# Kernel optimization log

Hardware: AMD Instinct MI355X
Metric: run time of the kernel (lower is better)

Reference implementation:

```python
import jax, jax.numpy as jnp
import numpy as np

N_NODES = 50000
N_EDGES = 1600000
IN_CH = 128
HID = 128
LAT = 32


def _sage_conv(h, src, dst, W_l, W_r, b, num_nodes):
    # PyG SAGEConv: mean-aggregate neighbor (source) features at dst,
    # then lin_l(aggr) + lin_r(x) + bias
    msg = h[src]                                             # [E, d] irregular gather
    agg = jax.ops.segment_sum(msg, dst, num_segments=num_nodes)
    cnt = jax.ops.segment_sum(jnp.ones((src.shape[0], 1), h.dtype), dst,
                              num_segments=num_nodes)
    mean = agg / jnp.maximum(cnt, 1.0)
    return mean @ W_l + h @ W_r + b


def setup_inputs() -> dict:
    key = jax.random.key(0)
    ks = jax.random.split(key, 16)
    s = 0.05
    inp = {
        "x": jax.random.normal(ks[0], (N_NODES, IN_CH), jnp.float32),
        "edge_index": jax.random.randint(ks[1], (2, N_EDGES), 0, N_NODES, jnp.int32),
        "eps": jax.random.normal(ks[2], (N_NODES, LAT), jnp.float32),
        # SAGEConv layer 0
        "Wl0": jax.random.normal(ks[3], (IN_CH, HID), jnp.float32) * s,
        "Wr0": jax.random.normal(ks[4], (IN_CH, HID), jnp.float32) * s,
        "b0": jnp.zeros((HID,), jnp.float32),
        # SAGEConv layer 1
        "Wl1": jax.random.normal(ks[5], (HID, HID), jnp.float32) * s,
        "Wr1": jax.random.normal(ks[6], (HID, HID), jnp.float32) * s,
        "b1": jnp.zeros((HID,), jnp.float32),
        # mu / logvar heads
        "Wmu": jax.random.normal(ks[7], (HID, LAT), jnp.float32) * s,
        "bmu": jnp.zeros((LAT,), jnp.float32),
        "Wlv": jax.random.normal(ks[8], (HID, LAT), jnp.float32) * s,
        "blv": jnp.zeros((LAT,), jnp.float32),
    }
    return inp


def reference(x, edge_index, eps, Wl0, Wr0, b0, Wl1, Wr1, b1, Wmu, bmu, Wlv, blv):
    src, dst = edge_index[0], edge_index[1]
    n = x.shape[0]
    h = jax.nn.relu(_sage_conv(x, src, dst, Wl0, Wr0, b0, n))
    h = jax.nn.relu(_sage_conv(h, src, dst, Wl1, Wr1, b1, n))
    mu = h @ Wmu + bmu
    logvar = h @ Wlv + blv
    z = mu + eps * jnp.exp(0.5 * logvar)          # reparameterize
    probs = jax.nn.sigmoid(jnp.sum(z[src] * z[dst], axis=-1))  # edge decode
    return probs, mu, logvar
```

## Files before the change

### kernel.cpp

```cpp
#include <hip/hip_runtime.h>
#include <math.h>

#define NN 50000
#define NE 1600000
#define CH 128
#define LAT 32
#define NB 196

__device__ __forceinline__ unsigned short f2bf(float f) {
  unsigned int u = __float_as_uint(f);
  unsigned int r = u + 0x7FFFu + ((u >> 16) & 1u);
  return (unsigned short)(r >> 16);
}
__device__ __forceinline__ float bf2f(unsigned short s) {
  return __uint_as_float(((unsigned int)s) << 16);
}

__global__ void k_tobf16(const float* __restrict__ in, unsigned short* __restrict__ out,
                         int n4) {
  int i = blockIdx.x * 256 + threadIdx.x;
  if (i < n4) {
    float4 v = reinterpret_cast<const float4*>(in)[i];
    ushort4 o;
    o.x = f2bf(v.x); o.y = f2bf(v.y); o.z = f2bf(v.z); o.w = f2bf(v.w);
    reinterpret_cast<ushort4*>(out)[i] = o;
  }
}

__global__ void k_hist(const int* __restrict__ dst, int* __restrict__ deg) {
  int e = blockIdx.x * 256 + threadIdx.x;
  if (e < NE) atomicAdd(&deg[dst[e]], 1);
}

__global__ void k_scan1(const int* __restrict__ deg, int* __restrict__ bsum) {
  __shared__ int red[256];
  int i = blockIdx.x * 256 + threadIdx.x;
  red[threadIdx.x] = (i < NN) ? deg[i] : 0;
  __syncthreads();
  for (int s = 128; s > 0; s >>= 1) {
    if (threadIdx.x < s) red[threadIdx.x] += red[threadIdx.x + s];
    __syncthreads();
  }
  if (threadIdx.x == 0) bsum[blockIdx.x] = red[0];
}

__global__ void k_scan2(const int* __restrict__ bsum, int* __restrict__ boff) {
  __shared__ int tmp[256];
  int t = threadIdx.x;
  int v = (t < NB) ? bsum[t] : 0;
  tmp[t] = v;
  __syncthreads();
  for (int off = 1; off < 256; off <<= 1) {
    int add = (t >= off) ? tmp[t - off] : 0;
    __syncthreads();
    tmp[t] += add;
    __syncthreads();
  }
  if (t < NB) boff[t] = tmp[t] - v;
}

__global__ void k_scan3(const int* __restrict__ deg, const int* __restrict__ boff,
                        int* __restrict__ row_start, int* __restrict__ cursor) {
  __shared__ int tmp[256];
  int t = threadIdx.x;
  int i = blockIdx.x * 256 + t;
  int v = (i < NN) ? deg[i] : 0;
  tmp[t] = v;
  __syncthreads();
  for (int off = 1; off < 256; off <<= 1) {
    int add = (t >= off) ? tmp[t - off] : 0;
    __syncthreads();
    tmp[t] += add;
    __syncthreads();
  }
  int excl = tmp[t] - v + boff[blockIdx.x];
  if (i < NN) { row_start[i] = excl; cursor[i] = excl; }
}

__global__ void k_fill(const int* __restrict__ src, const int* __restrict__ dst,
                       int* __restrict__ cursor, int* __restrict__ eid) {
  int e = blockIdx.x * 256 + threadIdx.x;
  if (e < NE) {
    int d = dst[e];
    int pos = atomicAdd(&cursor[d], 1);
    eid[pos] = src[e];
  }
}

__global__ __launch_bounds__(256) void k_sage2(
    const unsigned short* __restrict__ featb, const float* __restrict__ feat32,
    const int* __restrict__ deg, const int* __restrict__ row_start,
    const int* __restrict__ eid,
    const float* __restrict__ Wl, const float* __restrict__ Wr,
    const float* __restrict__ bias,
    float* __restrict__ outf, unsigned short* __restrict__ outb) {
  __shared__ float mean_s[32][128];
  __shared__ float h_s[32][128];
  int tid = threadIdx.x;
  int nbase = blockIdx.x * 32;
  int hw = tid >> 5, q = tid & 31;

  for (int n = hw; n < 32; n += 8) {
    int v = nbase + n;
    float ax = 0.f, ay = 0.f, az = 0.f, aw = 0.f;
    float4 hh = make_float4(0.f, 0.f, 0.f, 0.f);
    if (v < NN) {
      int r0 = row_start[v];
      int dg = deg[v];
      int i = 0;
      for (; i + 3 < dg; i += 4) {
        int s0 = eid[r0 + i + 0];
        int s1 = eid[r0 + i + 1];
        int s2 = eid[r0 + i + 2];
        int s3 = eid[r0 + i + 3];
        ushort4 a = *reinterpret_cast<const ushort4*>(featb + (size_t)s0 * CH + q * 4);
        ushort4 b = *reinterpret_cast<const ushort4*>(featb + (size_t)s1 * CH + q * 4);
        ushort4 c = *reinterpret_cast<const ushort4*>(featb + (size_t)s2 * CH + q * 4);
        ushort4 d = *reinterpret_cast<const ushort4*>(featb + (size_t)s3 * CH + q * 4);
        ax += bf2f(a.x) + bf2f(b.x) + bf2f(c.x) + bf2f(d.x);
        ay += bf2f(a.y) + bf2f(b.y) + bf2f(c.y) + bf2f(d.y);
        az += bf2f(a.z) + bf2f(b.z) + bf2f(c.z) + bf2f(d.z);
        aw += bf2f(a.w) + bf2f(b.w) + bf2f(c.w) + bf2f(d.w);
      }
      for (; i < dg; ++i) {
        int s0 = eid[r0 + i];
        ushort4 a = *reinterpret_cast<const ushort4*>(featb + (size_t)s0 * CH + q * 4);
        ax += bf2f(a.x); ay += bf2f(a.y); az += bf2f(a.z); aw += bf2f(a.w);
      }
      float r = 1.0f / (float)max(dg, 1);
      ax *= r; ay *= r; az *= r; aw *= r;
      if (feat32) {
        hh = *reinterpret_cast<const float4*>(feat32 + (size_t)v * CH + q * 4);
      } else {
        ushort4 hb = *reinterpret_cast<const ushort4*>(featb + (size_t)v * CH + q * 4);
        hh = make_float4(bf2f(hb.x), bf2f(hb.y), bf2f(hb.z), bf2f(hb.w));
      }
    }
    *reinterpret_cast<float4*>(&mean_s[n][q * 4]) = make_float4(ax, ay, az, aw);
    *reinterpret_cast<float4*>(&h_s[n][q * 4]) = hh;
  }
  __syncthreads();

  int jg = tid & 31, ng = tid >> 5;
  int j0 = jg * 4, nl = ng * 4;
  float acc[4][4];
#pragma unroll
  for (int a = 0; a < 4; a++)
#pragma unroll
    for (int b = 0; b < 4; b++) acc[a][b] = 0.f;

#pragma unroll 4
  for (int k = 0; k < 128; ++k) {
    float4 wl = *reinterpret_cast<const float4*>(Wl + k * CH + j0);
    float4 wr = *reinterpret_cast<const float4*>(Wr + k * CH + j0);
#pragma unroll
    for (int n = 0; n < 4; ++n) {
      float m = mean_s[nl + n][k];
      float hv = h_s[nl + n][k];
      acc[n][0] += m * wl.x + hv * wr.x;
      acc[n][1] += m * wl.y + hv * wr.y;
      acc[n][2] += m * wl.z + hv * wr.z;
      acc[n][3] += m * wl.w + hv * wr.w;
    }
  }

  float4 bb = *reinterpret_cast<const float4*>(bias + j0);
#pragma unroll
  for (int n = 0; n < 4; ++n) {
    int v = nbase + nl + n;
    if (v < NN) {
      float4 o;
      o.x = fmaxf(acc[n][0] + bb.x, 0.f);
      o.y = fmaxf(acc[n][1] + bb.y, 0.f);
      o.z = fmaxf(acc[n][2] + bb.z, 0.f);
      o.w = fmaxf(acc[n][3] + bb.w, 0.f);
      if (outf) *reinterpret_cast<float4*>(outf + (size_t)v * CH + j0) = o;
      if (outb) {
        ushort4 ob;
        ob.x = f2bf(o.x); ob.y = f2bf(o.y); ob.z = f2bf(o.z); ob.w = f2bf(o.w);
        *reinterpret_cast<ushort4*>(outb + (size_t)v * CH + j0) = ob;
      }
    }
  }
}

__global__ __launch_bounds__(256) void k_heads(
    const float* __restrict__ h2, const float* __restrict__ eps,
    const float* __restrict__ Wmu, const float* __restrict__ bmu,
    const float* __restrict__ Wlv, const float* __restrict__ blv,
    float* __restrict__ mu_out, float* __restrict__ lv_out,
    float* __restrict__ z) {
  __shared__ float hs[32][132];
  int tid = threadIdx.x;
  int nbase = blockIdx.x * 32;

  for (int f = tid; f < 1024; f += 256) {
    int row = f >> 5;
    int c4 = (f & 31) * 4;
    int v = nbase + row;
    float4 hh = make_float4(0.f, 0.f, 0.f, 0.f);
    if (v < NN) hh = *reinterpret_cast<const float4*>(h2 + (size_t)v * CH + c4);
    *reinterpret_cast<float4*>(&hs[row][c4]) = hh;
  }
  __syncthreads();

  int n = tid >> 3;
  int j0 = (tid & 7) * 4;
  float am[4] = {0.f, 0.f, 0.f, 0.f};
  float al[4] = {0.f, 0.f, 0.f, 0.f};
#pragma unroll 4
  for (int k = 0; k < 128; ++k) {
    float4 wm = *reinterpret_cast<const float4*>(Wmu + k * LAT + j0);
    float4 wv = *reinterpret_cast<const float4*>(Wlv + k * LAT + j0);
    float hv = hs[n][k];
    am[0] += hv * wm.x; am[1] += hv * wm.y; am[2] += hv * wm.z; am[3] += hv * wm.w;
    al[0] += hv * wv.x; al[1] += hv * wv.y; al[2] += hv * wv.z; al[3] += hv * wv.w;
  }
  int v = nbase + n;
  if (v < NN) {
    float4 bm = *reinterpret_cast<const float4*>(bmu + j0);
    float4 bl = *reinterpret_cast<const float4*>(blv + j0);
    float4 e4 = *reinterpret_cast<const float4*>(eps + (size_t)v * LAT + j0);
    float4 mu, lv, zz;
    mu.x = am[0] + bm.x; mu.y = am[1] + bm.y; mu.z = am[2] + bm.z; mu.w = am[3] + bm.w;
    lv.x = al[0] + bl.x; lv.y = al[1] + bl.y; lv.z = al[2] + bl.z; lv.w = al[3] + bl.w;
    zz.x = mu.x + e4.x * expf(0.5f * lv.x);
    zz.y = mu.y + e4.y * expf(0.5f * lv.y);
    zz.z = mu.z + e4.z * expf(0.5f * lv.z);
    zz.w = mu.w + e4.w * expf(0.5f * lv.w);
    *reinterpret_cast<float4*>(mu_out + (size_t)v * LAT + j0) = mu;
    *reinterpret_cast<float4*>(lv_out + (size_t)v * LAT + j0) = lv;
    *reinterpret_cast<float4*>(z + (size_t)v * LAT + j0) = zz;
  }
}

__global__ void k_decode(const int* __restrict__ src, const int* __restrict__ dst,
                         const float* __restrict__ z, float* __restrict__ probs) {
  int t = blockIdx.x * 256 + threadIdx.x;
  int e = t >> 3, part = t & 7;
  if (e >= NE) return;
  int s = src[e], d = dst[e];
  float4 a = *reinterpret_cast<const float4*>(z + (size_t)s * LAT + part * 4);
  float4 b = *reinterpret_cast<const float4*>(z + (size_t)d * LAT + part * 4);
  float p = a.x * b.x + a.y * b.y + a.z * b.z + a.w * b.w;
  p += __shfl_xor(p, 1);
  p += __shfl_xor(p, 2);
  p += __shfl_xor(p, 4);
  if (part == 0) probs[e] = 1.0f / (1.0f + expf(-p));
}

extern "C" void kernel_launch(void* const* d_in, const int* in_sizes, int n_in,
                              void* d_out, int out_size, void* d_ws, size_t ws_size,
                              hipStream_t stream) {
  const float* x   = (const float*)d_in[0];
  const int*   ei  = (const int*)d_in[1];
  const float* eps = (const float*)d_in[2];
  const float* Wl0 = (const float*)d_in[3];
  const float* Wr0 = (const float*)d_in[4];
  const float* b0  = (const float*)d_in[5];
  const float* Wl1 = (const float*)d_in[6];
  const float* Wr1 = (const float*)d_in[7];
  const float* b1  = (const float*)d_in[8];
  const float* Wmu = (const float*)d_in[9];
  const float* bmu = (const float*)d_in[10];
  const float* Wlv = (const float*)d_in[11];
  const float* blv = (const float*)d_in[12];
  const int* src = ei;
  const int* dst = ei + NE;

  int* iws = (int*)d_ws;
  int* deg       = iws;
  int* row_start = deg + NN;
  int* cursor    = row_start + NN;
  int* bsum      = cursor + NN;
  int* boff      = bsum + 256;
  int* eid       = boff + 256;
  unsigned short* xb  = (unsigned short*)(eid + NE);
  unsigned short* h1b = xb + (size_t)NN * CH;
  float* h2 = (float*)(h1b + (size_t)NN * CH);
  float* z  = (float*)h1b;

  float* probs  = (float*)d_out;
  float* mu_out = probs + NE;
  float* lv_out = mu_out + NN * LAT;

  hipMemsetAsync(deg, 0, NN * sizeof(int), stream);

  k_tobf16<<<(NN * CH / 4 + 255) / 256, 256, 0, stream>>>(x, xb, NN * CH / 4);
  k_hist <<<(NE + 255) / 256, 256, 0, stream>>>(dst, deg);
  k_scan1<<<NB, 256, 0, stream>>>(deg, bsum);
  k_scan2<<<1, 256, 0, stream>>>(bsum, boff);
  k_scan3<<<NB, 256, 0, stream>>>(deg, boff, row_start, cursor);
  k_fill <<<(NE + 255) / 256, 256, 0, stream>>>(src, dst, cursor, eid);

  k_sage2<<<(NN + 31) / 32, 256, 0, stream>>>(xb, x, deg, row_start, eid,
                                              Wl0, Wr0, b0, nullptr, h1b);
  k_sage2<<<(NN + 31) / 32, 256, 0, stream>>>(h1b, nullptr, deg, row_start, eid,
                                              Wl1, Wr1, b1, h2, nullptr);

  k_heads<<<(NN + 31) / 32, 256, 0, stream>>>(h2, eps, Wmu, bmu, Wlv, blv,
                                              mu_out, lv_out, z);
  k_decode<<<(NE * 8 + 255) / 256, 256, 0, stream>>>(src, dst, z, probs);
}
```

Measured before the change: 664.3 us.

## Store h2 and z in bf16 and pack sage shared tiles as transposed bf16

The second-layer output h2 and the latent z are now stored in bf16 rather than fp32, which halves the bytes moved by the heads kernel and the edge-decode gather. In k_sage2 the shared-memory mean and self-feature tiles become transposed bf16 arrays. The GEMM loop can then read four node values with one 8-byte LDS load, and the block uses less LDS, which together with launch bounds of 8 blocks per CU is meant to raise occupancy. The cost is extra rounding of the layer inputs, h2 and z, which could affect accuracy against the fp32 reference.

Result: no change. 659.5 us (-0.7%).

```diff
diff --git a/kernel.cpp b/kernel.cpp
--- a/kernel.cpp
+++ b/kernel.cpp
@@ -14,6 +14,12 @@
 }
 __device__ __forceinline__ float bf2f(unsigned short s) {
   return __uint_as_float(((unsigned int)s) << 16);
+}
+__device__ __forceinline__ float bflo(unsigned int u) {
+  return __uint_as_float(u << 16);
+}
+__device__ __forceinline__ float bfhi(unsigned int u) {
+  return __uint_as_float(u & 0xffff0000u);
 }
 
 __global__ void k_tobf16(const float* __restrict__ in, unsigned short* __restrict__ out,
@@ -87,23 +93,23 @@
   }
 }
 
-__global__ __launch_bounds__(256) void k_sage2(
+__global__ __launch_bounds__(256, 8) void k_sage2(
     const unsigned short* __restrict__ featb, const float* __restrict__ feat32,
     const int* __restrict__ deg, const int* __restrict__ row_start,
     const int* __restrict__ eid,
     const float* __restrict__ Wl, const float* __restrict__ Wr,
-    const float* __restrict__ bias,
-    float* __restrict__ outf, unsigned short* __restrict__ outb) {
-  __shared__ float mean_s[32][128];
-  __shared__ float h_s[32][128];
+    const float* __restrict__ bias, unsigned short* __restrict__ outb) {
+  __shared__ __align__(16) unsigned short mean_t[128][36];
+  __shared__ __align__(16) unsigned short h_t[128][36];
   int tid = threadIdx.x;
   int nbase = blockIdx.x * 32;
   int hw = tid >> 5, q = tid & 31;
+  int q4 = q * 4;
 
   for (int n = hw; n < 32; n += 8) {
     int v = nbase + n;
     float ax = 0.f, ay = 0.f, az = 0.f, aw = 0.f;
-    float4 hh = make_float4(0.f, 0.f, 0.f, 0.f);
+    float hx = 0.f, hy = 0.f, hz = 0.f, hwv = 0.f;
     if (v < NN) {
       int r0 = row_start[v];
       int dg = deg[v];
@@ -113,10 +119,10 @@
         int s1 = eid[r0 + i + 1];
         int s2 = eid[r0 + i + 2];
         int s3 = eid[r0 + i + 3];
-        ushort4 a = *reinterpret_cast<const ushort4*>(featb + (size_t)s0 * CH + q * 4);
-        ushort4 b = *reinterpret_cast<const ushort4*>(featb + (size_t)s1 * CH + q * 4);
-        ushort4 c = *reinterpret_cast<const ushort4*>(featb + (size_t)s2 * CH + q * 4);
-        ushort4 d = *reinterpret_cast<const ushort4*>(featb + (size_t)s3 * CH + q * 4);
+        ushort4 a = *reinterpret_cast<const ushort4*>(featb + (size_t)s0 * CH + q4);
+        ushort4 b = *reinterpret_cast<const ushort4*>(featb + (size_t)s1 * CH + q4);
+        ushort4 c = *reinterpret_cast<const ushort4*>(featb + (size_t)s2 * CH + q4);
+        ushort4 d = *reinterpret_cast<const ushort4*>(featb + (size_t)s3 * CH + q4);
         ax += bf2f(a.x) + bf2f(b.x) + bf2f(c.x) + bf2f(d.x);
         ay += bf2f(a.y) + bf2f(b.y) + bf2f(c.y) + bf2f(d.y);
         az += bf2f(a.z) + bf2f(b.z) + bf2f(c.z) + bf2f(d.z);
@@ -124,20 +130,27 @@
       }
       for (; i < dg; ++i) {
         int s0 = eid[r0 + i];
-        ushort4 a = *reinterpret_cast<const ushort4*>(featb + (size_t)s0 * CH + q * 4);
+        ushort4 a = *reinterpret_cast<const ushort4*>(featb + (size_t)s0 * CH + q4);
         ax += bf2f(a.x); ay += bf2f(a.y); az += bf2f(a.z); aw += bf2f(a.w);
       }
       float r = 1.0f / (float)max(dg, 1);
       ax *= r; ay *= r; az *= r; aw *= r;
       if (feat32) {
-        hh = *reinterpret_cast<const float4*>(feat32 + (size_t)v * CH + q * 4);
+        float4 hh = *reinterpret_cast<const float4*>(feat32 + (size_t)v * CH + q4);
+        hx = hh.x; hy = hh.y; hz = hh.z; hwv = hh.w;
       } else {
-        ushort4 hb = *reinterpret_cast<const ushort4*>(featb + (size_t)v * CH + q * 4);
-        hh = make_float4(bf2f(hb.x), bf2f(hb.y), bf2f(hb.z), bf2f(hb.w));
+        ushort4 hb = *reinterpret_cast<const ushort4*>(featb + (size_t)v * CH + q4);
+        hx = bf2f(hb.x); hy = bf2f(hb.y); hz = bf2f(hb.z); hwv = bf2f(hb.w);
       }
     }
-    *reinterpret_cast<float4*>(&mean_s[n][q * 4]) = make_float4(ax, ay, az, aw);
-    *reinterpret_cast<float4*>(&h_s[n][q * 4]) = hh;
+    mean_t[q4 + 0][n] = f2bf(ax);
+    mean_t[q4 + 1][n] = f2bf(ay);
+    mean_t[q4 + 2][n] = f2bf(az);
+    mean_t[q4 + 3][n] = f2bf(aw);
+    h_t[q4 + 0][n] = f2bf(hx);
+    h_t[q4 + 1][n] = f2bf(hy);
+    h_t[q4 + 2][n] = f2bf(hz);
+    h_t[q4 + 3][n] = f2bf(hwv);
   }
   __syncthreads();
 
@@ -149,18 +162,20 @@
 #pragma unroll
     for (int b = 0; b < 4; b++) acc[a][b] = 0.f;
 
-#pragma unroll 4
+#pragma unroll 2
   for (int k = 0; k < 128; ++k) {
     float4 wl = *reinterpret_cast<const float4*>(Wl + k * CH + j0);
     float4 wr = *reinterpret_cast<const float4*>(Wr + k * CH + j0);
+    uint2 mp = *reinterpret_cast<const uint2*>(&mean_t[k][nl]);
+    uint2 hp = *reinterpret_cast<const uint2*>(&h_t[k][nl]);
+    float mn[4] = {bflo(mp.x), bfhi(mp.x), bflo(mp.y), bfhi(mp.y)};
+    float hn[4] = {bflo(hp.x), bfhi(hp.x), bflo(hp.y), bfhi(hp.y)};
 #pragma unroll
     for (int n = 0; n < 4; ++n) {
-      float m = mean_s[nl + n][k];
-      float hv = h_s[nl + n][k];
-      acc[n][0] += m * wl.x + hv * wr.x;
-      acc[n][1] += m * wl.y + hv * wr.y;
-      acc[n][2] += m * wl.z + hv * wr.z;
-      acc[n][3] += m * wl.w + hv * wr.w;
+      acc[n][0] += mn[n] * wl.x + hn[n] * wr.x;
+      acc[n][1] += mn[n] * wl.y + hn[n] * wr.y;
+      acc[n][2] += mn[n] * wl.z + hn[n] * wr.z;
+      acc[n][3] += mn[n] * wl.w + hn[n] * wr.w;
     }
   }
 
@@ -169,27 +184,22 @@
   for (int n = 0; n < 4; ++n) {
     int v = nbase + nl + n;
     if (v < NN) {
-      float4 o;
-      o.x = fmaxf(acc[n][0] + bb.x, 0.f);
-      o.y = fmaxf(acc[n][1] + bb.y, 0.f);
-      o.z = fmaxf(acc[n][2] + bb.z, 0.f);
-      o.w = fmaxf(acc[n][3] + bb.w, 0.f);
-      if (outf) *reinterpret_cast<float4*>(outf + (size_t)v * CH + j0) = o;
-      if (outb) {
-        ushort4 ob;
-        ob.x = f2bf(o.x); ob.y = f2bf(o.y); ob.z = f2bf(o.z); ob.w = f2bf(o.w);
-        *reinterpret_cast<ushort4*>(outb + (size_t)v * CH + j0) = ob;
-      }
+      ushort4 ob;
+      ob.x = f2bf(fmaxf(acc[n][0] + bb.x, 0.f));
+      ob.y = f2bf(fmaxf(acc[n][1] + bb.y, 0.f));
+      ob.z = f2bf(fmaxf(acc[n][2] + bb.z, 0.f));
+      ob.w = f2bf(fmaxf(acc[n][3] + bb.w, 0.f));
+      *reinterpret_cast<ushort4*>(outb + (size_t)v * CH + j0) = ob;
     }
   }
 }
 
 __global__ __launch_bounds__(256) void k_heads(
-    const float* __restrict__ h2, const float* __restrict__ eps,
+    const unsigned short* __restrict__ h2b, const float* __restrict__ eps,
     const float* __restrict__ Wmu, const float* __restrict__ bmu,
     const float* __restrict__ Wlv, const float* __restrict__ blv,
     float* __restrict__ mu_out, float* __restrict__ lv_out,
-    float* __restrict__ z) {
+    unsigned short* __restrict__ zb) {
   __shared__ float hs[32][132];
   int tid = threadIdx.x;
   int nbase = blockIdx.x * 32;
@@ -199,7 +209,10 @@
     int c4 = (f & 31) * 4;
     int v = nbase + row;
     float4 hh = make_float4(0.f, 0.f, 0.f, 0.f);
-    if (v < NN) hh = *reinterpret_cast<const float4*>(h2 + (size_t)v * CH + c4);
+    if (v < NN) {
+      ushort4 hb = *reinterpret_cast<const ushort4*>(h2b + (size_t)v * CH + c4);
+      hh = make_float4(bf2f(hb.x), bf2f(hb.y), bf2f(hb.z), bf2f(hb.w));
+    }
     *reinterpret_cast<float4*>(&hs[row][c4]) = hh;
   }
   __syncthreads();
@@ -221,28 +234,31 @@
     float4 bm = *reinterpret_cast<const float4*>(bmu + j0);
     float4 bl = *reinterpret_cast<const float4*>(blv + j0);
     float4 e4 = *reinterpret_cast<const float4*>(eps + (size_t)v * LAT + j0);
-    float4 mu, lv, zz;
+    float4 mu, lv;
     mu.x = am[0] + bm.x; mu.y = am[1] + bm.y; mu.z = am[2] + bm.z; mu.w = am[3] + bm.w;
     lv.x = al[0] + bl.x; lv.y = al[1] + bl.y; lv.z = al[2] + bl.z; lv.w = al[3] + bl.w;
-    zz.x = mu.x + e4.x * expf(0.5f * lv.x);
-    zz.y = mu.y + e4.y * expf(0.5f * lv.y);
-    zz.z = mu.z + e4.z * expf(0.5f * lv.z);
-    zz.w = mu.w + e4.w * expf(0.5f * lv.w);
+    ushort4 zz;
+    zz.x = f2bf(mu.x + e4.x * expf(0.5f * lv.x));
+    zz.y = f2bf(mu.y + e4.y * expf(0.5f * lv.y));
+    zz.z = f2bf(mu.z + e4.z * expf(0.5f * lv.z));
+    zz.w = f2bf(mu.w + e4.w * expf(0.5f * lv.w));
     *reinterpret_cast<float4*>(mu_out + (size_t)v * LAT + j0) = mu;
     *reinterpret_cast<float4*>(lv_out + (size_t)v * LAT + j0) = lv;
-    *reinterpret_cast<float4*>(z + (size_t)v * LAT + j0) = zz;
+    *reinterpret_cast<ushort4*>(zb + (size_t)v * LAT + j0) = zz;
   }
 }
 
 __global__ void k_decode(const int* __restrict__ src, const int* __restrict__ dst,
-                         const float* __restrict__ z, float* __restrict__ probs) {
+                         const unsigned short* __restrict__ zb,
+                         float* __restrict__ probs) {
   int t = blockIdx.x * 256 + threadIdx.x;
   int e = t >> 3, part = t & 7;
   if (e >= NE) return;
   int s = src[e], d = dst[e];
-  float4 a = *reinterpret_cast<const float4*>(z + (size_t)s * LAT + part * 4);
-  float4 b = *reinterpret_cast<const float4*>(z + (size_t)d * LAT + part * 4);
-  float p = a.x * b.x + a.y * b.y + a.z * b.z + a.w * b.w;
+  ushort4 a = *reinterpret_cast<const ushort4*>(zb + (size_t)s * LAT + part * 4);
+  ushort4 b = *reinterpret_cast<const ushort4*>(zb + (size_t)d * LAT + part * 4);
+  float p = bf2f(a.x) * bf2f(b.x) + bf2f(a.y) * bf2f(b.y) +
+            bf2f(a.z) * bf2f(b.z) + bf2f(a.w) * bf2f(b.w);
   p += __shfl_xor(p, 1);
   p += __shfl_xor(p, 2);
   p += __shfl_xor(p, 4);
@@ -277,8 +293,8 @@
   int* eid       = boff + 256;
   unsigned short* xb  = (unsigned short*)(eid + NE);
   unsigned short* h1b = xb + (size_t)NN * CH;
-  float* h2 = (float*)(h1b + (size_t)NN * CH);
-  float* z  = (float*)h1b;
+  unsigned short* h2b = h1b + (size_t)NN * CH;
+  unsigned short* zb  = xb;
 
   float* probs  = (float*)d_out;
   float* mu_out = probs + NE;
@@ -294,11 +310,11 @@
   k_fill <<<(NE + 255) / 256, 256, 0, stream>>>(src, dst, cursor, eid);
 
   k_sage2<<<(NN + 31) / 32, 256, 0, stream>>>(xb, x, deg, row_start, eid,
-                                              Wl0, Wr0, b0, nullptr, h1b);
+                                              Wl0, Wr0, b0, h1b);
   k_sage2<<<(NN + 31) / 32, 256, 0, stream>>>(h1b, nullptr, deg, row_start, eid,
-                                              Wl1, Wr1, b1, h2, nullptr);
-
-  k_heads<<<(NN + 31) / 32, 256, 0, stream>>>(h2, eps, Wmu, bmu, Wlv, blv,
-                                              mu_out, lv_out, z);
-  k_decode<<<(NE * 8 + 255) / 256, 256, 0, stream>>>(src, dst, z, probs);
-}
+                                              Wl1, Wr1, b1, h2b);
+
+  k_heads<<<(NN + 31) / 32, 256, 0, stream>>>(h2b, eps, Wmu, bmu, Wlv, blv,
+                                              mu_out, lv_out, zb);
+  k_decode<<<(NE * 8 + 255) / 256, 256, 0, stream>>>(src, dst, zb, probs);
+}
```
